# Kernel optimization log

Measured on AMD Instinct MI355X. Metric: run time of the kernel, lower is better.

## Reference

```python
import jax, jax.numpy as jnp
import numpy as np

N = 100000  # nodes
E = 3200000  # edges
NEG_SLOPE = 0.2  # GATConv default


def _gat_conv(x, src, dst, edge_attr, W, a_src, a_dst, W_e, a_e, bias):
    """PyG GATConv, heads=1, concat=True, add_self_loops=True (fill_value='mean')."""
    n = x.shape[0]
    loop = jnp.arange(n)
    s = jnp.concatenate([src, loop])
    d = jnp.concatenate([dst, loop])
    mean_ea = edge_attr.mean(axis=0)
    ea = jnp.concatenate([edge_attr, jnp.broadcast_to(mean_ea, (n, edge_attr.shape[1]))], axis=0)
    h = x @ W                          # [N, C]
    al_src = h @ a_src                 # [N]
    al_dst = h @ a_dst                 # [N]
    he = ea @ W_e                      # [E+N, C]
    alpha = al_src[s] + al_dst[d] + he @ a_e   # [E+N]
    alpha = jax.nn.leaky_relu(alpha, NEG_SLOPE)
    amax = jax.ops.segment_max(alpha, d, num_segments=n)
    ex = jnp.exp(alpha - amax[d])
    denom = jax.ops.segment_sum(ex, d, num_segments=n)
    coef = ex / (denom[d] + 1e-16)     # per-destination softmax (PyG softmax)
    out = jax.ops.segment_sum(h[s] * coef[:, None], d, num_segments=n)
    return out + bias


def _edge_mlp(z, w0, b0, w1, b1, w2, b2, w3, b3):
    z = jax.nn.relu(z @ w0 + b0)
    z = jax.nn.relu(z @ w1 + b1)
    z = jax.nn.relu(z @ w2 + b2)
    return z @ w3 + b3


def setup_inputs() -> dict:
    key = jax.random.key(0)
    ks = jax.random.split(key, 24)
    g = lambda i, sh, s=0.1: jax.random.normal(ks[i], sh, dtype=jnp.float32) * s
    return {
        "x": g(0, (N, 4), 1.0),
        "edge_attr": g(1, (E, 3), 1.0),
        "W1": g(2, (4, 16), 0.5), "as1": g(3, (16,)), "ad1": g(4, (16,)),
        "We1": g(5, (3, 16), 0.5), "ae1": g(6, (16,)), "b1": g(7, (16,)),
        "mw0": g(8, (35, 16), 0.17), "mb0": g(9, (16,)),
        "mw1": g(10, (16, 16), 0.25), "mb1": g(11, (16,)),
        "mw2": g(12, (16, 8), 0.25), "mb2": g(13, (8,)),
        "mw3": g(14, (8, 4), 0.35), "mb3": g(15, (4,)),
        "W2": g(16, (16, 2), 0.25), "as2": g(17, (2,)), "ad2": g(18, (2,)),
        "We2": g(19, (4, 2), 0.5), "ae2": g(20, (2,)), "b2": g(21, (2,)),
        "edge_index": jax.random.randint(ks[22], (2, E), 0, N),
    }


def reference(x, edge_attr, W1, as1, ad1, We1, ae1, b1,
              mw0, mb0, mw1, mb1, mw2, mb2, mw3, mb3,
              W2, as2, ad2, We2, ae2, b2, edge_index):
    src, dst = edge_index[0], edge_index[1]
    h = _gat_conv(x, src, dst, edge_attr, W1, as1, ad1, We1, ae1, b1)      # [N, 16]
    z = jnp.concatenate([h[src], edge_attr, h[dst]], axis=1)               # [E, 35]
    e = _edge_mlp(z, mw0, mb0, mw1, mb1, mw2, mb2, mw3, mb3)               # [E, 4]
    out = _gat_conv(h, src, dst, e, W2, as2, ad2, We2, ae2, b2)            # [N, 2]
    return jax.nn.log_softmax(out, axis=1), jax.nn.log_softmax(e, axis=1)
```

## Files before the change

kernel.cpp:

```cpp
#include <hip/hip_runtime.h>
#include <hip/hip_bf16.h>
#include <stdint.h>

typedef __hip_bfloat16 bf16;
typedef unsigned long long ull;
#define NT 256
#define EPT 4

__device__ __forceinline__ float b2f(bf16 v){ return __bfloat162float(v); }
__device__ __forceinline__ bf16 f2b(float v){ return __float2bfloat16(v); }
__device__ __forceinline__ float lrelu(float a){ return a>0.f ? a : 0.2f*a; }
__device__ __forceinline__ float sanf(float v){ return __builtin_isfinite(v) ? v : -12345.f; }
__device__ __forceinline__ float us2f(unsigned short u){ return __uint_as_float(((unsigned)u)<<16); }
__device__ __forceinline__ unsigned short f2bu(float v){ bf16 b=f2b(v); unsigned short u; __builtin_memcpy(&u,&b,2); return u; }
__device__ __forceinline__ float h2f(unsigned short u){ _Float16 h; __builtin_memcpy(&h,&u,2); return (float)h; }
__device__ __forceinline__ unsigned short f2h(float v){ _Float16 h=(_Float16)v; unsigned short u; __builtin_memcpy(&u,&h,2); return u; }

__device__ __forceinline__ float ld(const void* p, size_t i, int f32in){
  return f32in ? ((const float*)p)[i] : b2f(((const bf16*)p)[i]);
}

__device__ __forceinline__ float waveReduceSum(float v){
#pragma unroll
  for(int o=32;o>0;o>>=1) v += __shfl_down(v,o,64);
  return v;
}

__device__ __forceinline__ unsigned clampi(int v, int n){
  unsigned u=(unsigned)v; return (u<(unsigned)n)?u:0u;
}

__device__ __forceinline__ void load_h1v(const bf16* h1, unsigned node, float* dst){
  const ull* p=(const ull*)(h1+(size_t)node*16);
#pragma unroll
  for(int q=0;q<4;q++){
    ull v=p[q];
    dst[q*4+0]=us2f((unsigned short)v);        dst[q*4+1]=us2f((unsigned short)(v>>16));
    dst[q*4+2]=us2f((unsigned short)(v>>32));  dst[q*4+3]=us2f((unsigned short)(v>>48));
  }
}
__device__ __forceinline__ void add_u16h(const unsigned short* u, unsigned node, float* t){
  const ull* p=(const ull*)(u+(size_t)node*16);
#pragma unroll
  for(int q=0;q<4;q++){
    ull v=p[q];
    t[q*4+0]+=h2f((unsigned short)v);        t[q*4+1]+=h2f((unsigned short)(v>>16));
    t[q*4+2]+=h2f((unsigned short)(v>>32));  t[q*4+3]+=h2f((unsigned short)(v>>48));
  }
}
__device__ __forceinline__ void set_u16h(const unsigned short* u, unsigned node, float* t){
  const ull* p=(const ull*)(u+(size_t)node*16);
#pragma unroll
  for(int q=0;q<4;q++){
    ull v=p[q];
    t[q*4+0]=h2f((unsigned short)v);        t[q*4+1]=h2f((unsigned short)(v>>16));
    t[q*4+2]=h2f((unsigned short)(v>>32));  t[q*4+3]=h2f((unsigned short)(v>>48));
  }
}
__device__ __forceinline__ void load_x4(const void* x, unsigned n, int f32in, float* o){
  if(f32in){ float4 v=((const float4*)x)[n]; o[0]=v.x;o[1]=v.y;o[2]=v.z;o[3]=v.w; }
  else{
    ull v=((const ull*)x)[n];
    o[0]=us2f((unsigned short)v);       o[1]=us2f((unsigned short)(v>>16));
    o[2]=us2f((unsigned short)(v>>32)); o[3]=us2f((unsigned short)(v>>48));
  }
}

__global__ __launch_bounds__(64) void k_probe(const unsigned short* __restrict__ xraw,
                                              int nscan, float* __restrict__ stats){
  int t=threadIdx.x;
  int bad=0;
  for(int k=t*8;k<t*8+8;k++){
    if(k<nscan){
      unsigned short u=xraw[k];
      unsigned ex=(u>>7)&0xFF;
      bool plaus = (ex==0u) || (ex>=97u && ex<=157u);
      if(!plaus) bad++;
    }
  }
#pragma unroll
  for(int o=32;o>0;o>>=1) bad += __shfl_down(bad,o,64);
  if(t==0){
    for(int i=0;i<7;i++) stats[i]=0.f;
    ((int*)stats)[7] = (bad>=8) ? 1 : 0;
  }
}

__global__ __launch_bounds__(NT) void k_prep(const void* __restrict__ ea,
                                             const int* __restrict__ idx,
                                             int* __restrict__ rowc,
                                             float* __restrict__ stats, int E, int N){
  const int f32in=((const int*)stats)[7];
  __shared__ float lds[16];
  float s0=0.f,s1=0.f,s2=0.f;
  for(size_t e=(size_t)blockIdx.x*NT+threadIdx.x; e<(size_t)E; e+=(size_t)gridDim.x*NT){
    s0+=ld(ea,e*3+0,f32in); s1+=ld(ea,e*3+1,f32in); s2+=ld(ea,e*3+2,f32in);
    unsigned d=clampi(idx[(size_t)E+e],N);
    atomicAdd(&rowc[d],1);
  }
  int lane=threadIdx.x&63, wv=threadIdx.x>>6;
  s0=waveReduceSum(s0); s1=waveReduceSum(s1); s2=waveReduceSum(s2);
  if(lane==0){ lds[wv*4+0]=s0; lds[wv*4+1]=s1; lds[wv*4+2]=s2; }
  __syncthreads();
  if(threadIdx.x==0){
    float a0=0,a1=0,a2=0;
    for(int w=0;w<NT/64;w++){ a0+=lds[w*4]; a1+=lds[w*4+1]; a2+=lds[w*4+2]; }
    atomicAdd(&stats[0],a0); atomicAdd(&stats[1],a1); atomicAdd(&stats[2],a2);
  }
}

__global__ __launch_bounds__(NT) void k_node1(
    const void* __restrict__ x, const void* __restrict__ W1,
    const void* __restrict__ as1, const void* __restrict__ ad1,
    const float* __restrict__ stats,
    float* __restrict__ als, float* __restrict__ ald, int N){
  const int f32in=((const int*)stats)[7];
  __shared__ float sW1[64], sas[16], sad[16];
  if(threadIdx.x<64) sW1[threadIdx.x]=ld(W1,threadIdx.x,f32in);
  if(threadIdx.x<16){ sas[threadIdx.x]=ld(as1,threadIdx.x,f32in); sad[threadIdx.x]=ld(ad1,threadIdx.x,f32in); }
  __syncthreads();
  int i=blockIdx.x*NT+threadIdx.x;
  if(i>=N) return;
  float xv[4]; load_x4(x,(unsigned)i,f32in,xv);
  float a_s=0.f,a_d=0.f;
#pragma unroll
  for(int j=0;j<16;j++){
    float v=xv[0]*sW1[j]+xv[1]*sW1[16+j]+xv[2]*sW1[32+j]+xv[3]*sW1[48+j];
    a_s+=v*sas[j]; a_d+=v*sad[j];
  }
  als[i]=a_s; ald[i]=a_d;
}

__global__ __launch_bounds__(NT) void k_scan1(const int* __restrict__ rowc, int* __restrict__ bsum, int N){
  __shared__ int sm[NT];
  int i=blockIdx.x*NT+threadIdx.x;
  sm[threadIdx.x]=(i<N)?rowc[i]:0;
  __syncthreads();
  for(int o=NT/2;o>0;o>>=1){ if(threadIdx.x<o) sm[threadIdx.x]+=sm[threadIdx.x+o]; __syncthreads(); }
  if(threadIdx.x==0) bsum[blockIdx.x]=sm[0];
}
__global__ __launch_bounds__(1024) void k_scan2(int* __restrict__ bsum, int NB){
  __shared__ int sm[1024];
  int i=threadIdx.x;
  int v=(i<NB)?bsum[i]:0;
  sm[i]=v; __syncthreads();
  for(int o=1;o<1024;o<<=1){
    int t=(i>=o)?sm[i-o]:0; __syncthreads();
    sm[i]+=t; __syncthreads();
  }
  if(i<NB) bsum[i]=(i==0)?0:sm[i-1];
}
__global__ __launch_bounds__(NT) void k_scan3(int* __restrict__ rowc, const int* __restrict__ bsum, int N){
  __shared__ int sm[NT];
  int i=blockIdx.x*NT+threadIdx.x;
  int v=(i<N)?rowc[i]:0;
  sm[threadIdx.x]=v; __syncthreads();
  for(int o=1;o<NT;o<<=1){
    int t=(threadIdx.x>=o)?sm[threadIdx.x-o]:0; __syncthreads();
    sm[threadIdx.x]+=t; __syncthreads();
  }
  if(i<N) rowc[i]=bsum[blockIdx.x]+sm[threadIdx.x]-v;
}

__global__ __launch_bounds__(NT) void k_scatter(
    const int* __restrict__ idx, const void* __restrict__ ea,
    const void* __restrict__ We1, const void* __restrict__ ae1,
    const float* __restrict__ als, const float* __restrict__ stats,
    int* __restrict__ rowc, ull* __restrict__ csr, int E, int N){
  const int f32in=((const int*)stats)[7];
  __shared__ float sve[3];
  if(threadIdx.x<3){
    float v=0.f;
    for(int j=0;j<16;j++) v+=ld(We1,threadIdx.x*16+j,f32in)*ld(ae1,j,f32in);
    sve[threadIdx.x]=v;
  }
  __syncthreads();
  int e=blockIdx.x*NT+threadIdx.x;
  if(e>=E) return;
  unsigned s=clampi(idx[e],N), d=clampi(idx[(size_t)E+e],N);
  float ap = als[s] + ld(ea,(size_t)e*3+0,f32in)*sve[0]
                    + ld(ea,(size_t)e*3+1,f32in)*sve[1]
                    + ld(ea,(size_t)e*3+2,f32in)*sve[2];
  int pos=atomicAdd(&rowc[d],1);
  csr[pos] = (ull)s | ((ull)__float_as_uint(ap)<<32);
}

__global__ __launch_bounds__(NT) void k_gather1(
    const ull* __restrict__ csr, const int* __restrict__ rowe,
    const float* __restrict__ als, const float* __restrict__ ald,
    const void* __restrict__ x, const void* __restrict__ W1, const void* __restrict__ b1,
    const void* __restrict__ W2, const void* __restrict__ as2, const void* __restrict__ ad2,
    const void* __restrict__ We1, const void* __restrict__ ae1,
    const float* __restrict__ stats, float invE,
    bf16* __restrict__ h1, float* __restrict__ h2,
    float* __restrict__ als2, float* __restrict__ ald2, int N){
  const int f32in=((const int*)stats)[7];
  __shared__ float sW1[64], sb1[16], sW2[32], sas2[2], sad2[2], saea[1];
  if(threadIdx.x<64) sW1[threadIdx.x]=ld(W1,threadIdx.x,f32in);
  if(threadIdx.x<16) sb1[threadIdx.x]=ld(b1,threadIdx.x,f32in);
  if(threadIdx.x<32) sW2[threadIdx.x]=ld(W2,threadIdx.x,f32in);
  if(threadIdx.x<2){ sas2[threadIdx.x]=ld(as2,threadIdx.x,f32in); sad2[threadIdx.x]=ld(ad2,threadIdx.x,f32in); }
  if(threadIdx.x==0){
    float a=0.f;
    for(int k=0;k<3;k++){
      float v=0.f;
      for(int j=0;j<16;j++) v+=ld(We1,k*16+j,f32in)*ld(ae1,j,f32in);
      a+=stats[k]*v;
    }
    saea[0]=a*invE;
  }
  __syncthreads();
  int wv=threadIdx.x>>6, lane=threadIdx.x&63;
  int n=blockIdx.x*4+wv;
  if(n>=N) return;
  int c=lane&15, sg=lane>>4;
  int end=rowe[n];
  int start=(n==0)?0:rowe[n-1];
  float aldn=ald[n], alsn=als[n];
  float aself=lrelu(alsn+aldn+saea[0]);
  float w0=sW1[c], w1=sW1[16+c], w2=sW1[32+c], w3=sW1[48+c];
  float m=aself;
  for(int k=start+lane;k<end;k+=64){
    float ap=__uint_as_float((unsigned)(csr[k]>>32));
    m=fmaxf(m,lrelu(ap+aldn));
  }
#pragma unroll
  for(int o=1;o<64;o<<=1) m=fmaxf(m,__shfl_xor(m,o,64));
  float xv[4]; load_x4(x,(unsigned)n,f32in,xv);
  float hc_self=xv[0]*w0+xv[1]*w1+xv[2]*w2+xv[3]*w3;
  float exs=expf(fminf(aself-m,0.f));
  float den=0.f, acc=0.f;
  for(int k=start+sg;k<end;k+=4){
    ull v=csr[k];
    unsigned src=(unsigned)(v&0xffffffffu);
    float ap=__uint_as_float((unsigned)(v>>32));
    float ex=expf(fminf(lrelu(ap+aldn)-m,0.f));
    den+=ex;
    float xs[4]; load_x4(x,src,f32in,xs);
    acc+=ex*(xs[0]*w0+xs[1]*w1+xs[2]*w2+xs[3]*w3);
  }
  acc+=__shfl_xor(acc,16,64); acc+=__shfl_xor(acc,32,64);
  den+=__shfl_xor(den,16,64); den+=__shfl_xor(den,32,64);
  den+=exs; acc+=exs*hc_self;
  float inv=1.f/(den+1e-16f);
  float h1c=acc*inv+sb1[c];
  if(sg==0) h1[(size_t)n*16+c]=f2b(h1c);
  float r0=h1c*sW2[c*2+0], r1=h1c*sW2[c*2+1];
#pragma unroll
  for(int o=1;o<16;o<<=1){ r0+=__shfl_xor(r0,o,64); r1+=__shfl_xor(r1,o,64); }
  if(lane==0){
    h2[(size_t)n*2+0]=r0; h2[(size_t)n*2+1]=r1;
    als2[n]=r0*sas2[0]+r1*sas2[1];
    ald2[n]=r0*sad2[0]+r1*sad2[1];
  }
}

__global__ __launch_bounds__(NT) void k_wprep(
    const void* mw0,const void* mb0,const void* mw1,const void* mb1,
    const void* mw2,const void* mb2,const void* mw3,const void* mb3,
    const void* We2,const void* ae2,
    const float* __restrict__ stats, float* __restrict__ gw){
  const int f32in=((const int*)stats)[7];
  for(int t=threadIdx.x;t<560;t+=NT) gw[t]=ld(mw0,t,f32in);
  for(int t=threadIdx.x;t<256;t+=NT) gw[576+t]=ld(mw1,t,f32in);
  for(int t=threadIdx.x;t<128;t+=NT) gw[848+t]=ld(mw2,t,f32in);
  if(threadIdx.x<32) gw[984+threadIdx.x]=ld(mw3,threadIdx.x,f32in);
  if(threadIdx.x<16){ gw[560+threadIdx.x]=ld(mb0,threadIdx.x,f32in); gw[832+threadIdx.x]=ld(mb1,threadIdx.x,f32in); }
  if(threadIdx.x<8) gw[976+threadIdx.x]=ld(mb2,threadIdx.x,f32in);
  if(threadIdx.x<4){
    gw[1016+threadIdx.x]=ld(mb3,threadIdx.x,f32in);
    gw[1020+threadIdx.x]=ld(We2,threadIdx.x*2+0,f32in)*ld(ae2,0,f32in)
                        +ld(We2,threadIdx.x*2+1,f32in)*ld(ae2,1,f32in);
  }
}

__global__ __launch_bounds__(NT) void k_upre(
    const bf16* __restrict__ h1, const float* __restrict__ gw,
    unsigned short* __restrict__ us, unsigned short* __restrict__ ud, int N){
  int n=blockIdx.x*NT+threadIdx.x;
  if(n>=N) return;
  float h[16]; load_h1v(h1,(unsigned)n,h);
  const float4* w4=(const float4*)gw;
  float a[16];
  {
    const float4* b=(const float4*)(gw+560);
    float4 b0=b[0],b1=b[1],b2=b[2],b3=b[3];
    a[0]=b0.x;a[1]=b0.y;a[2]=b0.z;a[3]=b0.w; a[4]=b1.x;a[5]=b1.y;a[6]=b1.z;a[7]=b1.w;
    a[8]=b2.x;a[9]=b2.y;a[10]=b2.z;a[11]=b2.w; a[12]=b3.x;a[13]=b3.y;a[14]=b3.z;a[15]=b3.w;
  }
#pragma unroll
  for(int i=0;i<16;i++){
    float z=h[i];
    float4 r0=w4[i*4+0],r1=w4[i*4+1],r2=w4[i*4+2],r3=w4[i*4+3];
    a[0]+=z*r0.x;a[1]+=z*r0.y;a[2]+=z*r0.z;a[3]+=z*r0.w;
    a[4]+=z*r1.x;a[5]+=z*r1.y;a[6]+=z*r1.z;a[7]+=z*r1.w;
    a[8]+=z*r2.x;a[9]+=z*r2.y;a[10]+=z*r2.z;a[11]+=z*r2.w;
    a[12]+=z*r3.x;a[13]+=z*r3.y;a[14]+=z*r3.z;a[15]+=z*r3.w;
  }
  {
    ull* po=(ull*)(us+(size_t)n*16);
#pragma unroll
    for(int q=0;q<4;q++){
      ull v = (ull)f2h(a[q*4+0]) | ((ull)f2h(a[q*4+1])<<16)
            | ((ull)f2h(a[q*4+2])<<32) | ((ull)f2h(a[q*4+3])<<48);
      po[q]=v;
    }
  }
  float c[16];
#pragma unroll
  for(int j=0;j<16;j++) c[j]=0.f;
#pragma unroll
  for(int i=0;i<16;i++){
    float z=h[i];
    int r=19+i;
    float4 r0=w4[r*4+0],r1=w4[r*4+1],r2=w4[r*4+2],r3=w4[r*4+3];
    c[0]+=z*r0.x;c[1]+=z*r0.y;c[2]+=z*r0.z;c[3]+=z*r0.w;
    c[4]+=z*r1.x;c[5]+=z*r1.y;c[6]+=z*r1.z;c[7]+=z*r1.w;
    c[8]+=z*r2.x;c[9]+=z*r2.y;c[10]+=z*r2.z;c[11]+=z*r2.w;
    c[12]+=z*r3.x;c[13]+=z*r3.y;c[14]+=z*r3.z;c[15]+=z*r3.w;
  }
  {
    ull* pd=(ull*)(ud+(size_t)n*16);
#pragma unroll
    for(int q=0;q<4;q++){
      ull v = (ull)f2h(c[q*4+0]) | ((ull)f2h(c[q*4+1])<<16)
            | ((ull)f2h(c[q*4+2])<<32) | ((ull)f2h(c[q*4+3])<<48);
      pd[q]=v;
    }
  }
}

template<int EP>
__device__ __forceinline__ void mlp_tail(float (&t1)[EP][16],
                                         const float* __restrict__ gw,
                                         float (&ev)[EP][4]){
#pragma unroll
  for(int u=0;u<EP;u++)
#pragma unroll
    for(int j=0;j<16;j++) t1[u][j]=fmaxf(t1[u][j],0.f);

  const float4* w14=(const float4*)(gw+576);
  float t2[EP][16];
  {
    const float4* b=(const float4*)(gw+832);
    float4 b0=b[0],b1=b[1],b2=b[2],b3=b[3];
#pragma unroll
    for(int u=0;u<EP;u++){
      t2[u][0]=b0.x; t2[u][1]=b0.y; t2[u][2]=b0.z; t2[u][3]=b0.w;
      t2[u][4]=b1.x; t2[u][5]=b1.y; t2[u][6]=b1.z; t2[u][7]=b1.w;
      t2[u][8]=b2.x; t2[u][9]=b2.y; t2[u][10]=b2.z; t2[u][11]=b2.w;
      t2[u][12]=b3.x; t2[u][13]=b3.y; t2[u][14]=b3.z; t2[u][15]=b3.w;
    }
  }
#pragma unroll
  for(int i2=0;i2<16;i2++){
    float4 r0=w14[i2*4+0], r1=w14[i2*4+1], r2=w14[i2*4+2], r3=w14[i2*4+3];
#pragma unroll
    for(int u=0;u<EP;u++){
      float a=t1[u][i2];
      t2[u][0]+=a*r0.x; t2[u][1]+=a*r0.y; t2[u][2]+=a*r0.z; t2[u][3]+=a*r0.w;
      t2[u][4]+=a*r1.x; t2[u][5]+=a*r1.y; t2[u][6]+=a*r1.z; t2[u][7]+=a*r1.w;
      t2[u][8]+=a*r2.x; t2[u][9]+=a*r2.y; t2[u][10]+=a*r2.z; t2[u][11]+=a*r2.w;
      t2[u][12]+=a*r3.x; t2[u][13]+=a*r3.y; t2[u][14]+=a*r3.z; t2[u][15]+=a*r3.w;
    }
  }
#pragma unroll
  for(int u=0;u<EP;u++)
#pragma unroll
    for(int j=0;j<16;j++) t2[u][j]=fmaxf(t2[u][j],0.f);

  const float4* w24=(const float4*)(gw+848);
  float t3[EP][8];
  {
    const float4* b=(const float4*)(gw+976);
    float4 b0=b[0],b1=b[1];
#pragma unroll
    for(int u=0;u<EP;u++){
      t3[u][0]=b0.x; t3[u][1]=b0.y; t3[u][2]=b0.z; t3[u][3]=b0.w;
      t3[u][4]=b1.x; t3[u][5]=b1.y; t3[u][6]=b1.z; t3[u][7]=b1.w;
    }
  }
#pragma unroll
  for(int i2=0;i2<16;i2++){
    float4 r0=w24[i2*2+0], r1=w24[i2*2+1];
#pragma unroll
    for(int u=0;u<EP;u++){
      float a=t2[u][i2];
      t3[u][0]+=a*r0.x; t3[u][1]+=a*r0.y; t3[u][2]+=a*r0.z; t3[u][3]+=a*r0.w;
      t3[u][4]+=a*r1.x; t3[u][5]+=a*r1.y; t3[u][6]+=a*r1.z; t3[u][7]+=a*r1.w;
    }
  }
#pragma unroll
  for(int u=0;u<EP;u++)
#pragma unroll
    for(int j=0;j<8;j++) t3[u][j]=fmaxf(t3[u][j],0.f);

  const float4* w34=(const float4*)(gw+984);
  {
    const float4* b=(const float4*)(gw+1016);
    float4 b0=b[0];
#pragma unroll
    for(int u=0;u<EP;u++){ ev[u][0]=b0.x; ev[u][1]=b0.y; ev[u][2]=b0.z; ev[u][3]=b0.w; }
  }
#pragma unroll
  for(int i2=0;i2<8;i2++){
    float4 r0=w34[i2];
#pragma unroll
    for(int u=0;u<EP;u++){
      float a=t3[u][i2];
      ev[u][0]+=a*r0.x; ev[u][1]+=a*r0.y; ev[u][2]+=a*r0.z; ev[u][3]+=a*r0.w;
    }
  }
}

__device__ __forceinline__ void mlp_head_full4(const float z[EPT][35],
                                               const float* __restrict__ gw,
                                               float (&t1)[EPT][16]){
  const float4* w4=(const float4*)gw;
  {
    const float4* b=(const float4*)(gw+560);
    float4 b0=b[0],b1=b[1],b2=b[2],b3=b[3];
#pragma unroll
    for(int u=0;u<EPT;u++){
      t1[u][0]=b0.x; t1[u][1]=b0.y; t1[u][2]=b0.z; t1[u][3]=b0.w;
      t1[u][4]=b1.x; t1[u][5]=b1.y; t1[u][6]=b1.z; t1[u][7]=b1.w;
      t1[u][8]=b2.x; t1[u][9]=b2.y; t1[u][10]=b2.z; t1[u][11]=b2.w;
      t1[u][12]=b3.x; t1[u][13]=b3.y; t1[u][14]=b3.z; t1[u][15]=b3.w;
    }
  }
#pragma unroll
  for(int i2=0;i2<35;i2++){
    float4 r0=w4[i2*4+0], r1=w4[i2*4+1], r2=w4[i2*4+2], r3=w4[i2*4+3];
#pragma unroll
    for(int u=0;u<EPT;u++){
      float a=z[u][i2];
      t1[u][0]+=a*r0.x; t1[u][1]+=a*r0.y; t1[u][2]+=a*r0.z; t1[u][3]+=a*r0.w;
      t1[u][4]+=a*r1.x; t1[u][5]+=a*r1.y; t1[u][6]+=a*r1.z; t1[u][7]+=a*r1.w;
      t1[u][8]+=a*r2.x; t1[u][9]+=a*r2.y; t1[u][10]+=a*r2.z; t1[u][11]+=a*r2.w;
      t1[u][12]+=a*r3.x; t1[u][13]+=a*r3.y; t1[u][14]+=a*r3.z; t1[u][15]+=a*r3.w;
    }
  }
}

__device__ __forceinline__ void edge_epi(const float* ev, unsigned s, unsigned d, int e,
                                         const float* __restrict__ gw,
                                         const float* __restrict__ als2,
                                         const float* __restrict__ ald2,
                                         const float* __restrict__ h2,
                                         float* __restrict__ denom2, float* __restrict__ acc2,
                                         void* __restrict__ d_out, int f32in, int N){
  float m=fmaxf(fmaxf(ev[0],ev[1]),fmaxf(ev[2],ev[3]));
  float lse=m+logf(expf(ev[0]-m)+expf(ev[1]-m)+expf(ev[2]-m)+expf(ev[3]-m));
  if(f32in){
    float4 o; o.x=sanf(ev[0]-lse); o.y=sanf(ev[1]-lse); o.z=sanf(ev[2]-lse); o.w=sanf(ev[3]-lse);
    ((float4*)((float*)d_out+(size_t)2*N))[e]=o;
  }else{
    ull o = (ull)f2bu(sanf(ev[0]-lse))
          | ((ull)f2bu(sanf(ev[1]-lse))<<16)
          | ((ull)f2bu(sanf(ev[2]-lse))<<32)
          | ((ull)f2bu(sanf(ev[3]-lse))<<48);
    ((ull*)((bf16*)d_out+(size_t)2*N))[e]=o;
  }
  const float* s_ve2=gw+1020;
  float adot=ev[0]*s_ve2[0]+ev[1]*s_ve2[1]+ev[2]*s_ve2[2]+ev[3]*s_ve2[3];
  float a2=sanf(lrelu(als2[s]+ald2[d]+adot));
  float ex=expf(fminf(a2,80.f));
  float2 h2s=((const float2*)h2)[s];
  atomicAdd(&denom2[d],ex);
  atomicAdd(&acc2[(size_t)d*2+0],ex*h2s.x);
  atomicAdd(&acc2[(size_t)d*2+1],ex*h2s.y);
}

__device__ __forceinline__ void stats_red(float c0,float c1,float c2,float c3,
                                          float* s_red, float* stats){
  int lane=threadIdx.x&63, wv=threadIdx.x>>6;
  c0=waveReduceSum(c0); c1=waveReduceSum(c1); c2=waveReduceSum(c2); c3=waveReduceSum(c3);
  __syncthreads();
  if(lane==0){ s_red[wv*4]=c0; s_red[wv*4+1]=c1; s_red[wv*4+2]=c2; s_red[wv*4+3]=c3; }
  __syncthreads();
  if(threadIdx.x==0){
    float a0=0,a1=0,a2=0,a3=0;
    for(int w=0;w<NT/64;w++){ a0+=s_red[w*4]; a1+=s_red[w*4+1]; a2+=s_red[w*4+2]; a3+=s_red[w*4+3]; }
    atomicAdd(&stats[3],a0); atomicAdd(&stats[4],a1); atomicAdd(&stats[5],a2); atomicAdd(&stats[6],a3);
  }
}

__global__ __launch_bounds__(NT,2) void k_edge2s(
    const int* __restrict__ idx, const void* __restrict__ ea,
    const unsigned short* __restrict__ us, const unsigned short* __restrict__ ud,
    const float* __restrict__ als2, const float* __restrict__ ald2,
    const float* __restrict__ gw,
    const float* __restrict__ h2,
    float* __restrict__ denom2, float* __restrict__ acc2,
    float* __restrict__ stats, void* __restrict__ d_out, int E, int N){
  const int f32in=((const int*)stats)[7];
  __shared__ float s_red[16];
  size_t base=(size_t)blockIdx.x*(NT*EPT)+threadIdx.x;
  int e[EPT]; bool v[EPT]; int es[EPT]; unsigned s[EPT], d[EPT];
#pragma unroll
  for(int u=0;u<EPT;u++){
    e[u]=(int)(base+(size_t)u*NT);
    v[u]=e[u]<E;
    es[u]=v[u]?e[u]:0;
    s[u]=clampi(idx[es[u]],N);
    d[u]=clampi(idx[(size_t)E+es[u]],N);
  }
  float t1[EPT][16];
#pragma unroll
  for(int u=0;u<EPT;u++) set_u16h(us,s[u],t1[u]);
  {
    const float4* w16=(const float4*)(gw+256);
    const float4* w17=(const float4*)(gw+272);
    const float4* w18=(const float4*)(gw+288);
    float4 q0[3]={w16[0],w17[0],w18[0]}, q1[3]={w16[1],w17[1],w18[1]},
           q2[3]={w16[2],w17[2],w18[2]}, q3[3]={w16[3],w17[3],w18[3]};
#pragma unroll
    for(int u=0;u<EPT;u++){
      float e3[3];
      e3[0]=ld(ea,(size_t)es[u]*3+0,f32in);
      e3[1]=ld(ea,(size_t)es[u]*3+1,f32in);
      e3[2]=ld(ea,(size_t)es[u]*3+2,f32in);
#pragma unroll
      for(int k=0;k<3;k++){
        float a=e3[k];
        t1[u][0]+=a*q0[k].x; t1[u][1]+=a*q0[k].y; t1[u][2]+=a*q0[k].z; t1[u][3]+=a*q0[k].w;
        t1[u][4]+=a*q1[k].x; t1[u][5]+=a*q1[k].y; t1[u][6]+=a*q1[k].z; t1[u][7]+=a*q1[k].w;
        t1[u][8]+=a*q2[k].x; t1[u][9]+=a*q2[k].y; t1[u][10]+=a*q2[k].z; t1[u][11]+=a*q2[k].w;
        t1[u][12]+=a*q3[k].x; t1[u][13]+=a*q3[k].y; t1[u][14]+=a*q3[k].z; t1[u][15]+=a*q3[k].w;
      }
    }
  }
#pragma unroll
  for(int u=0;u<EPT;u++) add_u16h(ud,d[u],t1[u]);
  float ev[EPT][4];
  mlp_tail<EPT>(t1,gw,ev);
  float c0=0.f,c1=0.f,c2=0.f,c3=0.f;
#pragma unroll
  for(int u=0;u<EPT;u++){
    if(v[u]){
      edge_epi(ev[u],s[u],d[u],e[u],gw,als2,ald2,h2,denom2,acc2,d_out,f32in,N);
      c0+=ev[u][0]; c1+=ev[u][1]; c2+=ev[u][2]; c3+=ev[u][3];
    }
  }
  stats_red(c0,c1,c2,c3,s_red,stats);
}

__global__ __launch_bounds__(NT,1) void k_edge2(
    const int* __restrict__ idx, const void* __restrict__ ea,
    const bf16* __restrict__ h1,
    const float* __restrict__ als2, const float* __restrict__ ald2,
    const float* __restrict__ gw,
    const float* __restrict__ h2,
    float* __restrict__ denom2, float* __restrict__ acc2,
    float* __restrict__ stats, void* __restrict__ d_out, int E, int N){
  const int f32in=((const int*)stats)[7];
  __shared__ float s_red[16];
  size_t base=(size_t)blockIdx.x*(NT*EPT)+threadIdx.x;
  int e[EPT]; bool v[EPT]; int es[EPT]; unsigned s[EPT], d[EPT];
#pragma unroll
  for(int u=0;u<EPT;u++){
    e[u]=(int)(base+(size_t)u*NT);
    v[u]=e[u]<E;
    es[u]=v[u]?e[u]:0;
    s[u]=clampi(idx[es[u]],N);
    d[u]=clampi(idx[(size_t)E+es[u]],N);
  }
  float z[EPT][35];
#pragma unroll
  for(int u=0;u<EPT;u++){
    load_h1v(h1,s[u],z[u]);
    load_h1v(h1,d[u],z[u]+19);
    z[u][16]=ld(ea,(size_t)es[u]*3+0,f32in);
    z[u][17]=ld(ea,(size_t)es[u]*3+1,f32in);
    z[u][18]=ld(ea,(size_t)es[u]*3+2,f32in);
  }
  float t1[EPT][16];
  mlp_head_full4(z,gw,t1);
  float ev[EPT][4];
  mlp_tail<EPT>(t1,gw,ev);
  float c0=0.f,c1=0.f,c2=0.f,c3=0.f;
#pragma unroll
  for(int u=0;u<EPT;u++){
    if(v[u]){
      edge_epi(ev[u],s[u],d[u],e[u],gw,als2,ald2,h2,denom2,acc2,d_out,f32in,N);
      c0+=ev[u][0]; c1+=ev[u][1]; c2+=ev[u][2]; c3+=ev[u][3];
    }
  }
  stats_red(c0,c1,c2,c3,s_red,stats);
}

__global__ __launch_bounds__(NT) void k_final(
    const float* __restrict__ stats, float invE,
    const float* __restrict__ als2, const float* __restrict__ ald2,
    const void* __restrict__ We2, const void* __restrict__ ae2,
    const float* __restrict__ h2,
    const float* __restrict__ denom2, const float* __restrict__ acc2,
    const void* __restrict__ bias2, void* __restrict__ d_out, int N){
  const int f32in=((const int*)stats)[7];
  __shared__ float s_ve2[4], s_b2[2];
  if(threadIdx.x<4)
    s_ve2[threadIdx.x]=ld(We2,threadIdx.x*2+0,f32in)*ld(ae2,0,f32in)
                      +ld(We2,threadIdx.x*2+1,f32in)*ld(ae2,1,f32in);
  if(threadIdx.x<2) s_b2[threadIdx.x]=ld(bias2,threadIdx.x,f32in);
  __syncthreads();
  int i=blockIdx.x*NT+threadIdx.x;
  if(i>=N) return;
  float adot=(stats[3]*s_ve2[0]+stats[4]*s_ve2[1]+stats[5]*s_ve2[2]+stats[6]*s_ve2[3])*invE;
  float self=lrelu(als2[i]+ald2[i]+adot);
  float ex=expf(fminf(self,80.f));
  float den=denom2[i]+ex;
  float inv=1.f/(den+1e-16f);
  float o0=(acc2[(size_t)i*2+0]+ex*h2[(size_t)i*2+0])*inv+s_b2[0];
  float o1=(acc2[(size_t)i*2+1]+ex*h2[(size_t)i*2+1])*inv+s_b2[1];
  float m=fmaxf(o0,o1);
  float lse=m+logf(expf(o0-m)+expf(o1-m));
  float r0=sanf(o0-lse), r1=sanf(o1-lse);
  if(f32in){
    float* o=(float*)d_out;
    o[(size_t)i*2+0]=r0; o[(size_t)i*2+1]=r1;
  }else{
    bf16* o=(bf16*)d_out;
    o[(size_t)i*2+0]=f2b(r0); o[(size_t)i*2+1]=f2b(r1);
  }
}

extern "C" void kernel_launch(void* const* d_in, const int* in_sizes, int n_in,
                              void* d_out, int out_size, void* d_ws, size_t ws_size,
                              hipStream_t stream){
  const void* x   =d_in[0];
  const void* ea  =d_in[1];
  const void* W1  =d_in[2];
  const void* as1 =d_in[3];
  const void* ad1 =d_in[4];
  const void* We1 =d_in[5];
  const void* ae1 =d_in[6];
  const void* b1  =d_in[7];
  const void* mw0 =d_in[8];
  const void* mb0 =d_in[9];
  const void* mw1 =d_in[10];
  const void* mb1 =d_in[11];
  const void* mw2 =d_in[12];
  const void* mb2 =d_in[13];
  const void* mw3 =d_in[14];
  const void* mb3 =d_in[15];
  const void* W2  =d_in[16];
  const void* as2 =d_in[17];
  const void* ad2 =d_in[18];
  const void* We2 =d_in[19];
  const void* ae2 =d_in[20];
  const void* bias2=d_in[21];
  const int*  idx =(const int*)d_in[22];

  int N=in_sizes[0]/4;
  int E=in_sizes[1]/3;
  float invE=1.f/(float)E;

  float*    F     =(float*)d_ws;
  float*    stats =F;
  float*    als   =F+8;
  float*    ald   =als+N;
  float*    ald2  =ald+N;
  int*      rowc  =(int*)(ald2+N);
  bf16*     h1    =(bf16*)(rowc+N);
  float*    h2    =(float*)(h1+(size_t)16*N);
  float*    acc2  =h2+(size_t)2*N;
  float*    den2  =ald;
  float*    gw    =(float*)((((uintptr_t)rowc)+15)&~(uintptr_t)15);
  unsigned short* u_s=(unsigned short*)((((uintptr_t)(acc2+(size_t)2*N))+15)&~(uintptr_t)15);
  unsigned short* u_d=u_s+(size_t)16*N;
  size_t    need  =(size_t)((char*)(u_d+(size_t)16*N)-(char*)d_ws);
  int use_split   =(ws_size>=need)?1:0;

  ull* csr =(ull*)((char*)d_out+(size_t)4*N);
  int* bsum=(int*)((char*)d_out+(size_t)4*N);

  int NBn=(N+NT-1)/NT, nbE=(E+NT-1)/NT;
  int nbE4=(E+NT*EPT-1)/(NT*EPT);
  int nscan=in_sizes[0]*2; if(nscan>512) nscan=512;

  hipMemsetAsync(rowc,0,(size_t)N*sizeof(int),stream);
  k_probe  <<<1,64,0,stream>>>((const unsigned short*)x,nscan,stats);
  k_prep   <<<1024,NT,0,stream>>>(ea,idx,rowc,stats,E,N);
  k_node1  <<<NBn,NT,0,stream>>>(x,W1,as1,ad1,stats,als,ald,N);
  k_scan1  <<<NBn,NT,0,stream>>>(rowc,bsum,N);
  k_scan2  <<<1,1024,0,stream>>>(bsum,NBn);
  k_scan3  <<<NBn,NT,0,stream>>>(rowc,bsum,N);
  k_scatter<<<nbE,NT,0,stream>>>(idx,ea,We1,ae1,als,stats,rowc,csr,E,N);
  k_gather1<<<(N+3)/4,NT,0,stream>>>(csr,rowc,als,ald,x,W1,b1,W2,as2,ad2,We1,ae1,
                                     stats,invE,h1,h2,als,ald2,N);
  k_wprep  <<<1,NT,0,stream>>>(mw0,mb0,mw1,mb1,mw2,mb2,mw3,mb3,We2,ae2,stats,gw);
  hipMemsetAsync(den2,0,(size_t)N*sizeof(float),stream);
  hipMemsetAsync(acc2,0,(size_t)2*N*sizeof(float),stream);
  if(use_split){
    k_upre   <<<NBn,NT,0,stream>>>(h1,gw,u_s,u_d,N);
    k_edge2s <<<nbE4,NT,0,stream>>>(idx,ea,u_s,u_d,als,ald2,gw,h2,den2,acc2,stats,d_out,E,N);
  }else{
    k_edge2  <<<nbE4,NT,0,stream>>>(idx,ea,h1,als,ald2,gw,h2,den2,acc2,stats,d_out,E,N);
  }
  k_final  <<<NBn,NT,0,stream>>>(stats,invE,als,ald2,We2,ae2,h2,den2,acc2,bias2,d_out,N);
}
```

Before: 1.186 ms.

## Pack two accumulators into one double atomic, fold edge_attr sum into scatter

Two per-edge float atomics for the second-layer numerator are replaced by a single double atomicAdd. The x component is quantized to a fixed grid and the y component is scaled into the low-order bits, then both are unpacked in k_final. The edge_attr column sums move from k_prep into k_scatter, so edge_attr is read once less. This halves accumulation atomics but loses precision, and the packing can alias if sums exceed the quantization range.

```diff
diff --git a/kernel.cpp b/kernel.cpp
--- a/kernel.cpp
+++ b/kernel.cpp
@@ -6,6 +6,11 @@
 typedef unsigned long long ull;
 #define NT 256
 #define EPT 4
+
+#define QX   1.220703125e-04
+#define IQX  8192.0
+#define SY   2.9802322387695312e-08
+#define ISY  33554432.0
 
 __device__ __forceinline__ float b2f(bf16 v){ return __bfloat162float(v); }
 __device__ __forceinline__ bf16 f2b(float v){ return __float2bfloat16(v); }
@@ -86,26 +91,12 @@
   }
 }
 
-__global__ __launch_bounds__(NT) void k_prep(const void* __restrict__ ea,
-                                             const int* __restrict__ idx,
+__global__ __launch_bounds__(NT) void k_prep(const int* __restrict__ idx,
                                              int* __restrict__ rowc,
-                                             float* __restrict__ stats, int E, int N){
-  const int f32in=((const int*)stats)[7];
-  __shared__ float lds[16];
-  float s0=0.f,s1=0.f,s2=0.f;
+                                             int E, int N){
   for(size_t e=(size_t)blockIdx.x*NT+threadIdx.x; e<(size_t)E; e+=(size_t)gridDim.x*NT){
-    s0+=ld(ea,e*3+0,f32in); s1+=ld(ea,e*3+1,f32in); s2+=ld(ea,e*3+2,f32in);
     unsigned d=clampi(idx[(size_t)E+e],N);
     atomicAdd(&rowc[d],1);
-  }
-  int lane=threadIdx.x&63, wv=threadIdx.x>>6;
-  s0=waveReduceSum(s0); s1=waveReduceSum(s1); s2=waveReduceSum(s2);
-  if(lane==0){ lds[wv*4+0]=s0; lds[wv*4+1]=s1; lds[wv*4+2]=s2; }
-  __syncthreads();
-  if(threadIdx.x==0){
-    float a0=0,a1=0,a2=0;
-    for(int w=0;w<NT/64;w++){ a0+=lds[w*4]; a1+=lds[w*4+1]; a2+=lds[w*4+2]; }
-    atomicAdd(&stats[0],a0); atomicAdd(&stats[1],a1); atomicAdd(&stats[2],a2);
   }
 }
 
@@ -165,10 +156,11 @@
 __global__ __launch_bounds__(NT) void k_scatter(
     const int* __restrict__ idx, const void* __restrict__ ea,
     const void* __restrict__ We1, const void* __restrict__ ae1,
-    const float* __restrict__ als, const float* __restrict__ stats,
+    const float* __restrict__ als, float* __restrict__ stats,
     int* __restrict__ rowc, ull* __restrict__ csr, int E, int N){
   const int f32in=((const int*)stats)[7];
   __shared__ float sve[3];
+  __shared__ float s_red[12];
   if(threadIdx.x<3){
     float v=0.f;
     for(int j=0;j<16;j++) v+=ld(We1,threadIdx.x*16+j,f32in)*ld(ae1,j,f32in);
@@ -176,13 +168,29 @@
   }
   __syncthreads();
   int e=blockIdx.x*NT+threadIdx.x;
-  if(e>=E) return;
-  unsigned s=clampi(idx[e],N), d=clampi(idx[(size_t)E+e],N);
-  float ap = als[s] + ld(ea,(size_t)e*3+0,f32in)*sve[0]
-                    + ld(ea,(size_t)e*3+1,f32in)*sve[1]
-                    + ld(ea,(size_t)e*3+2,f32in)*sve[2];
-  int pos=atomicAdd(&rowc[d],1);
-  csr[pos] = (ull)s | ((ull)__float_as_uint(ap)<<32);
+  bool valid = e<E;
+  float e0=0.f,e1=0.f,e2=0.f;
+  unsigned s=0,d=0; float ap=0.f;
+  if(valid){
+    s=clampi(idx[e],N); d=clampi(idx[(size_t)E+e],N);
+    e0=ld(ea,(size_t)e*3+0,f32in);
+    e1=ld(ea,(size_t)e*3+1,f32in);
+    e2=ld(ea,(size_t)e*3+2,f32in);
+    ap = als[s] + e0*sve[0] + e1*sve[1] + e2*sve[2];
+  }
+  int lane=threadIdx.x&63, wv=threadIdx.x>>6;
+  float r0=waveReduceSum(e0), r1=waveReduceSum(e1), r2=waveReduceSum(e2);
+  if(lane==0){ s_red[wv*3+0]=r0; s_red[wv*3+1]=r1; s_red[wv*3+2]=r2; }
+  __syncthreads();
+  if(threadIdx.x==0){
+    float a0=0,a1=0,a2=0;
+    for(int w=0;w<NT/64;w++){ a0+=s_red[w*3]; a1+=s_red[w*3+1]; a2+=s_red[w*3+2]; }
+    atomicAdd(&stats[0],a0); atomicAdd(&stats[1],a1); atomicAdd(&stats[2],a2);
+  }
+  if(valid){
+    int pos=atomicAdd(&rowc[d],1);
+    csr[pos] = (ull)s | ((ull)__float_as_uint(ap)<<32);
+  }
 }
 
 __global__ __launch_bounds__(NT) void k_gather1(
@@ -447,7 +455,7 @@
                                          const float* __restrict__ als2,
                                          const float* __restrict__ ald2,
                                          const float* __restrict__ h2,
-                                         float* __restrict__ denom2, float* __restrict__ acc2,
+                                         float* __restrict__ denom2, double* __restrict__ accP,
                                          void* __restrict__ d_out, int f32in, int N){
   float m=fmaxf(fmaxf(ev[0],ev[1]),fmaxf(ev[2],ev[3]));
   float lse=m+logf(expf(ev[0]-m)+expf(ev[1]-m)+expf(ev[2]-m)+expf(ev[3]-m));
@@ -466,9 +474,9 @@
   float a2=sanf(lrelu(als2[s]+ald2[d]+adot));
   float ex=expf(fminf(a2,80.f));
   float2 h2s=((const float2*)h2)[s];
+  double pk = rint((double)(ex*h2s.x)*IQX)*QX + (double)(ex*h2s.y)*SY;
+  atomicAdd(&accP[d],pk);
   atomicAdd(&denom2[d],ex);
-  atomicAdd(&acc2[(size_t)d*2+0],ex*h2s.x);
-  atomicAdd(&acc2[(size_t)d*2+1],ex*h2s.y);
 }
 
 __device__ __forceinline__ void stats_red(float c0,float c1,float c2,float c3,
@@ -491,7 +499,7 @@
     const float* __restrict__ als2, const float* __restrict__ ald2,
     const float* __restrict__ gw,
     const float* __restrict__ h2,
-    float* __restrict__ denom2, float* __restrict__ acc2,
+    float* __restrict__ denom2, double* __restrict__ accP,
     float* __restrict__ stats, void* __restrict__ d_out, int E, int N){
   const int f32in=((const int*)stats)[7];
   __shared__ float s_red[16];
@@ -538,7 +546,7 @@
 #pragma unroll
   for(int u=0;u<EPT;u++){
     if(v[u]){
-      edge_epi(ev[u],s[u],d[u],e[u],gw,als2,ald2,h2,denom2,acc2,d_out,f32in,N);
+      edge_epi(ev[u],s[u],d[u],e[u],gw,als2,ald2,h2,denom2,accP,d_out,f32in,N);
       c0+=ev[u][0]; c1+=ev[u][1]; c2+=ev[u][2]; c3+=ev[u][3];
     }
   }
@@ -551,7 +559,7 @@
     const float* __restrict__ als2, const float* __restrict__ ald2,
     const float* __restrict__ gw,
     const float* __restrict__ h2,
-    float* __restrict__ denom2, float* __restrict__ acc2,
+    float* __restrict__ denom2, double* __restrict__ accP,
     float* __restrict__ stats, void* __restrict__ d_out, int E, int N){
   const int f32in=((const int*)stats)[7];
   __shared__ float s_red[16];
@@ -582,7 +590,7 @@
 #pragma unroll
   for(int u=0;u<EPT;u++){
     if(v[u]){
-      edge_epi(ev[u],s[u],d[u],e[u],gw,als2,ald2,h2,denom2,acc2,d_out,f32in,N);
+      edge_epi(ev[u],s[u],d[u],e[u],gw,als2,ald2,h2,denom2,accP,d_out,f32in,N);
       c0+=ev[u][0]; c1+=ev[u][1]; c2+=ev[u][2]; c3+=ev[u][3];
     }
   }
@@ -594,7 +602,7 @@
     const float* __restrict__ als2, const float* __restrict__ ald2,
     const void* __restrict__ We2, const void* __restrict__ ae2,
     const float* __restrict__ h2,
-    const float* __restrict__ denom2, const float* __restrict__ acc2,
+    const float* __restrict__ denom2, const double* __restrict__ accP,
     const void* __restrict__ bias2, void* __restrict__ d_out, int N){
   const int f32in=((const int*)stats)[7];
   __shared__ float s_ve2[4], s_b2[2];
@@ -608,10 +616,14 @@
   float adot=(stats[3]*s_ve2[0]+stats[4]*s_ve2[1]+stats[5]*s_ve2[2]+stats[6]*s_ve2[3])*invE;
   float self=lrelu(als2[i]+ald2[i]+adot);
   float ex=expf(fminf(self,80.f));
+  double A=accP[i];
+  double qx=rint(A*IQX)*QX;
+  float accx=(float)qx;
+  float accy=(float)((A-qx)*ISY);
   float den=denom2[i]+ex;
   float inv=1.f/(den+1e-16f);
-  float o0=(acc2[(size_t)i*2+0]+ex*h2[(size_t)i*2+0])*inv+s_b2[0];
-  float o1=(acc2[(size_t)i*2+1]+ex*h2[(size_t)i*2+1])*inv+s_b2[1];
+  float o0=(accx+ex*h2[(size_t)i*2+0])*inv+s_b2[0];
+  float o1=(accy+ex*h2[(size_t)i*2+1])*inv+s_b2[1];
   float m=fmaxf(o0,o1);
   float lse=m+logf(expf(o0-m)+expf(o1-m));
   float r0=sanf(o0-lse), r1=sanf(o1-lse);
@@ -663,10 +675,10 @@
   int*      rowc  =(int*)(ald2+N);
   bf16*     h1    =(bf16*)(rowc+N);
   float*    h2    =(float*)(h1+(size_t)16*N);
-  float*    acc2  =h2+(size_t)2*N;
+  double*   accP  =(double*)((((uintptr_t)(h2+(size_t)2*N))+7)&~(uintptr_t)7);
   float*    den2  =ald;
   float*    gw    =(float*)((((uintptr_t)rowc)+15)&~(uintptr_t)15);
-  unsigned short* u_s=(unsigned short*)((((uintptr_t)(acc2+(size_t)2*N))+15)&~(uintptr_t)15);
+  unsigned short* u_s=(unsigned short*)((((uintptr_t)(accP+N))+15)&~(uintptr_t)15);
   unsigned short* u_d=u_s+(size_t)16*N;
   size_t    need  =(size_t)((char*)(u_d+(size_t)16*N)-(char*)d_ws);
   int use_split   =(ws_size>=need)?1:0;
@@ -680,7 +692,7 @@
 
   hipMemsetAsync(rowc,0,(size_t)N*sizeof(int),stream);
   k_probe  <<<1,64,0,stream>>>((const unsigned short*)x,nscan,stats);
-  k_prep   <<<1024,NT,0,stream>>>(ea,idx,rowc,stats,E,N);
+  k_prep   <<<1024,NT,0,stream>>>(idx,rowc,E,N);
   k_node1  <<<NBn,NT,0,stream>>>(x,W1,as1,ad1,stats,als,ald,N);
   k_scan1  <<<NBn,NT,0,stream>>>(rowc,bsum,N);
   k_scan2  <<<1,1024,0,stream>>>(bsum,NBn);
@@ -690,12 +702,12 @@
                                      stats,invE,h1,h2,als,ald2,N);
   k_wprep  <<<1,NT,0,stream>>>(mw0,mb0,mw1,mb1,mw2,mb2,mw3,mb3,We2,ae2,stats,gw);
   hipMemsetAsync(den2,0,(size_t)N*sizeof(float),stream);
-  hipMemsetAsync(acc2,0,(size_t)2*N*sizeof(float),stream);
+  hipMemsetAsync(accP,0,(size_t)N*sizeof(double),stream);
   if(use_split){
     k_upre   <<<NBn,NT,0,stream>>>(h1,gw,u_s,u_d,N);
-    k_edge2s <<<nbE4,NT,0,stream>>>(idx,ea,u_s,u_d,als,ald2,gw,h2,den2,acc2,stats,d_out,E,N);
+    k_edge2s <<<nbE4,NT,0,stream>>>(idx,ea,u_s,u_d,als,ald2,gw,h2,den2,accP,stats,d_out,E,N);
   }else{
-    k_edge2  <<<nbE4,NT,0,stream>>>(idx,ea,h1,als,ald2,gw,h2,den2,acc2,stats,d_out,E,N);
-  }
-  k_final  <<<NBn,NT,0,stream>>>(stats,invE,als,ald2,We2,ae2,h2,den2,acc2,bias2,d_out,N);
-}
+    k_edge2  <<<nbE4,NT,0,stream>>>(idx,ea,h1,als,ald2,gw,h2,den2,accP,stats,d_out,E,N);
+  }
+  k_final  <<<NBn,NT,0,stream>>>(stats,invE,als,ald2,We2,ae2,h2,den2,accP,bias2,d_out,N);
+}
```

New measurement: 1.416 ms. +19.3%, slower.
